# Kernel tuning notes

Hardware: AMD Instinct MI355X
Metric: run time of the kernel (lower is better)

The kernel has to match this reference:

```python
import jax, jax.numpy as jnp
import numpy as np

HIDDEN = 3072
HEADS = 24
HEAD_DIM = HIDDEN // HEADS  # 128
MLP_HIDDEN = 4 * HIDDEN     # 12288
EPS = 1e-6


def rotate_half(x):
    # interleaved pairs: (x1, x2) -> (-x2, x1)
    xr = x.reshape(*x.shape[:-1], -1, 2)
    x1, x2 = xr[..., 0], xr[..., 1]
    return jnp.stack((-x2, x1), axis=-1).reshape(x.shape)


def rms_norm(x, gamma):
    var = jnp.mean(x * x, axis=-1, keepdims=True)
    return x * jax.lax.rsqrt(var + EPS) * gamma


def layer_norm(x):
    mu = jnp.mean(x, axis=-1, keepdims=True)
    var = jnp.mean(jnp.square(x - mu), axis=-1, keepdims=True)
    return (x - mu) * jax.lax.rsqrt(var + EPS)


def setup_inputs() -> dict:
    key = jax.random.key(0)
    ks = jax.random.split(key, 8)
    B, L_IMG, TXT = 2, 1024, 256
    L = L_IMG + TXT
    s = 0.02
    x = jax.random.normal(ks[0], (B, L, HIDDEN), jnp.float32)
    vec = jax.random.normal(ks[1], (B, HIDDEN), jnp.float32)
    w1 = jax.random.normal(ks[2], (HIDDEN, 3 * HIDDEN + MLP_HIDDEN), jnp.float32) * s
    b1 = jnp.zeros((3 * HIDDEN + MLP_HIDDEN,), jnp.float32)
    w2 = jax.random.normal(ks[3], (HIDDEN + MLP_HIDDEN, HIDDEN), jnp.float32) * s
    b2 = jnp.zeros((HIDDEN,), jnp.float32)
    wmod = jax.random.normal(ks[4], (HIDDEN, 3 * HIDDEN), jnp.float32) * s
    bmod = jnp.zeros((3 * HIDDEN,), jnp.float32)
    q_gamma = jnp.ones((HEAD_DIM,), jnp.float32)
    k_gamma = jnp.ones((HEAD_DIM,), jnp.float32)
    # real RoPE tables for the image tokens
    inv_freq = 1.0 / (10000.0 ** (np.arange(0, HEAD_DIM, 2, dtype=np.float32) / HEAD_DIM))
    angles = np.arange(L_IMG, dtype=np.float32)[:, None] * inv_freq[None, :]  # [L_img, D/2]
    freqs_cos = jnp.asarray(np.repeat(np.cos(angles), 2, axis=-1))  # [L_img, D]
    freqs_sin = jnp.asarray(np.repeat(np.sin(angles), 2, axis=-1))
    cu_seqlens_q = jnp.asarray([0, L, L, 2 * L, 2 * L], jnp.int32)  # no padding
    return {"x": x, "vec": vec, "w1": w1, "b1": b1, "w2": w2, "b2": b2,
            "wmod": wmod, "bmod": bmod, "q_gamma": q_gamma, "k_gamma": k_gamma,
            "freqs_cos": freqs_cos, "freqs_sin": freqs_sin,
            "txt_len": TXT, "cu_seqlens_q": cu_seqlens_q}


def reference(x, vec, w1, b1, w2, b2, wmod, bmod, q_gamma, k_gamma,
              freqs_cos, freqs_sin, txt_len, cu_seqlens_q):
    B, L, _ = x.shape
    # modulation: SiLU(vec) @ Wmod -> shift/scale/gate
    mod = jax.nn.silu(vec) @ wmod + bmod              # [B, 3H]
    mod_shift, mod_scale, mod_gate = jnp.split(mod, 3, axis=-1)
    x_mod = layer_norm(x) * (1.0 + mod_scale[:, None, :]) + mod_shift[:, None, :]
    h = x_mod @ w1 + b1                               # [B, L, 3H + mlp]
    qkv, mlp = h[..., :3 * HIDDEN], h[..., 3 * HIDDEN:]
    qkv = qkv.reshape(B, L, 3, HEADS, HEAD_DIM)
    q, k, v = qkv[:, :, 0], qkv[:, :, 1], qkv[:, :, 2]  # [B, L, H, D]
    q = rms_norm(q, q_gamma)
    k = rms_norm(k, k_gamma)
    # RoPE on image tokens (first L - txt_len)
    cos = freqs_cos[None, :, None, :]
    sin = freqs_sin[None, :, None, :]
    img_q, txt_q = q[:, :-txt_len], q[:, -txt_len:]
    img_k, txt_k = k[:, :-txt_len], k[:, -txt_len:]
    img_q = img_q * cos + rotate_half(img_q) * sin
    img_k = img_k * cos + rotate_half(img_k) * sin
    q = jnp.concatenate((img_q, txt_q), axis=1)
    k = jnp.concatenate((img_k, txt_k), axis=1)
    # full attention (no padding => each batch is one varlen segment)
    scale = HEAD_DIM ** -0.5
    scores = jnp.einsum("bqhd,bkhd->bhqk", q, k) * scale
    probs = jax.nn.softmax(scores, axis=-1)
    attn = jnp.einsum("bhqk,bkhd->bqhd", probs, v).reshape(B, L, HIDDEN)
    out = jnp.concatenate((attn, jax.nn.gelu(mlp, approximate=True)), axis=-1) @ w2 + b2
    return x + out * mod_gate[:, None, :]
```

## Files before the change

kernel.cpp:

```cpp
#include <hip/hip_runtime.h>

typedef unsigned short u16;
typedef unsigned int   u32;
typedef __attribute__((ext_vector_type(2))) u16 u16x2;
typedef __attribute__((ext_vector_type(4))) u16 u16x4;
typedef __attribute__((ext_vector_type(8))) u16 u16x8;
typedef __attribute__((ext_vector_type(8))) __bf16 bf16x8;
typedef __attribute__((ext_vector_type(4))) float f32x4;

#define HIDDEN 3072
#define LTOT 1280
#define BATCH 2
#define NROWS (BATCH*LTOT)
#define HEADS 24
#define HD 128
#define N1 21504
#define QKVW 9216
#define MLPW 12288
#define A2W 15360
#define EPSF 1e-6f

__device__ __forceinline__ float b2f(u16 u) {
  union { u32 i; float f; } v; v.i = ((u32)u) << 16; return v.f;
}
__device__ __forceinline__ u16 f2b(float f) {
  union { float f; u32 i; } v; v.f = f;
  u32 r = (v.i + 0x7FFFu + ((v.i >> 16) & 1u)) >> 16;
  return (u16)r;
}
__device__ __forceinline__ float lde(const void* p, size_t i, int f) {
  return f ? b2f(((const u16*)p)[i]) : ((const float*)p)[i];
}
__device__ __forceinline__ void gload16(const void* g, void* l) {
  __builtin_amdgcn_global_load_lds((const __attribute__((address_space(1))) void*)g,
                                   (__attribute__((address_space(3))) void*)l, 16, 0, 0);
}
__device__ __forceinline__ bf16x8 ldf(const u16* p) {
  return __builtin_bit_cast(bf16x8, *(const u16x8*)p);
}
__device__ __forceinline__ float gelu_tanh(float x) {
  float u = 0.7978845608028654f * (x + 0.044715f * x * x * x);
  float e = __expf(2.0f * u);
  float th = 1.0f - 2.0f / (e + 1.0f);
  return 0.5f * x * (1.0f + th);
}

__global__ void detect_kernel(const u16* __restrict__ fcos, int* __restrict__ dflag) {
  if (threadIdx.x == 0 && blockIdx.x == 0) *dflag = (fcos[0] == 0x3F80) ? 1 : 0;
}

__global__ void silu_kernel(const void* __restrict__ vec, float* __restrict__ sv,
                            const int* __restrict__ dflag) {
  int flag = *dflag;
  int i = blockIdx.x * 256 + threadIdx.x;
  if (i < BATCH * HIDDEN) { float x = lde(vec, i, flag); sv[i] = x / (1.0f + __expf(-x)); }
}

__global__ void modmul(const void* __restrict__ wmod, const float* __restrict__ sv,
                       float* __restrict__ modp, const int* __restrict__ dflag) {
  int flag = *dflag;
  int j = blockIdx.x * 256 + threadIdx.x;
  int kc = blockIdx.y;
  float a = 0.f, c = 0.f;
  int k0 = kc * 384;
  for (int k = k0; k < k0 + 384; ++k) {
    float w = lde(wmod, (size_t)k * QKVW + j, flag);
    a += sv[k] * w; c += sv[HIDDEN + k] * w;
  }
  modp[(size_t)kc * 2 * QKVW + j] = a;
  modp[(size_t)kc * 2 * QKVW + QKVW + j] = c;
}

__global__ void modred(const float* __restrict__ modp, const void* __restrict__ bmod,
                       float* __restrict__ mod, const int* __restrict__ dflag) {
  int flag = *dflag;
  int j = blockIdx.x * 256 + threadIdx.x;
  float bv = lde(bmod, j, flag);
  float a = bv, c = bv;
#pragma unroll
  for (int kc = 0; kc < 8; ++kc) {
    a += modp[(size_t)kc * 2 * QKVW + j];
    c += modp[(size_t)kc * 2 * QKVW + QKVW + j];
  }
  mod[j] = a; mod[QKVW + j] = c;
}

__global__ __launch_bounds__(256) void ln_mod_kernel(const void* __restrict__ x,
                                                     const float* __restrict__ mod,
                                                     u16* __restrict__ xmod,
                                                     const int* __restrict__ dflag) {
  int flag = *dflag;
  int row = blockIdx.x;
  int b = row / LTOT;
  int t = threadIdx.x, w = t >> 6, l = t & 63;
  float v[12], sum = 0.0f, sq = 0.0f;
  if (flag) {
    const u16* xr = (const u16*)x + (size_t)row * HIDDEN;
#pragma unroll
    for (int p = 0; p < 3; ++p) {
      u16x4 u = *(const u16x4*)&xr[p * 1024 + t * 4];
#pragma unroll
      for (int i = 0; i < 4; ++i) { float f = b2f(u[i]); v[p * 4 + i] = f; sum += f; sq += f * f; }
    }
  } else {
    const float* xr = (const float*)x + (size_t)row * HIDDEN;
#pragma unroll
    for (int p = 0; p < 3; ++p) {
      f32x4 u = *(const f32x4*)&xr[p * 1024 + t * 4];
#pragma unroll
      for (int i = 0; i < 4; ++i) { float f = u[i]; v[p * 4 + i] = f; sum += f; sq += f * f; }
    }
  }
#pragma unroll
  for (int off = 1; off < 64; off <<= 1) { sum += __shfl_xor(sum, off, 64); sq += __shfl_xor(sq, off, 64); }
  __shared__ float red[2][4];
  if (l == 0) { red[0][w] = sum; red[1][w] = sq; }
  __syncthreads();
  sum = red[0][0] + red[0][1] + red[0][2] + red[0][3];
  sq  = red[1][0] + red[1][1] + red[1][2] + red[1][3];
  float mu = sum / (float)HIDDEN;
  float var = sq / (float)HIDDEN - mu * mu;
  float rs = rsqrtf(var + EPSF);
  const float* mb = mod + (size_t)b * QKVW;
#pragma unroll
  for (int p = 0; p < 3; ++p) {
    u16x4 o;
#pragma unroll
    for (int i = 0; i < 4; ++i) {
      int col = p * 1024 + t * 4 + i;
      float y = (v[p * 4 + i] - mu) * rs;
      o[i] = f2b(y * (1.0f + mb[HIDDEN + col]) + mb[col]);
    }
    *(u16x4*)&xmod[(size_t)row * HIDDEN + p * 1024 + t * 4] = o;
  }
}

__global__ void transpose_cvt(const void* __restrict__ in, u16* __restrict__ out,
                              int R, int C, const int* __restrict__ dflag) {
  int flag = *dflag;
  __shared__ u16 tile[32][33];
  int bx = blockIdx.x * 32, by = blockIdx.y * 32;
  int tx = threadIdx.x & 31, ty = threadIdx.x >> 5;
#pragma unroll
  for (int i = 0; i < 32; i += 8)
    tile[ty + i][tx] = f2b(lde(in, (size_t)(by + ty + i) * C + bx + tx, flag));
  __syncthreads();
#pragma unroll
  for (int i = 0; i < 32; i += 8) out[(size_t)(bx + ty + i) * R + by + tx] = tile[tx][ty + i];
}

__global__ void transpose_bf16(const u16* __restrict__ in, u16* __restrict__ out,
                               int R, int C, size_t ibs, size_t obs) {
  in  += (size_t)blockIdx.z * ibs;
  out += (size_t)blockIdx.z * obs;
  __shared__ u16 tile[32][33];
  int bx = blockIdx.x * 32, by = blockIdx.y * 32;
  int tx = threadIdx.x & 31, ty = threadIdx.x >> 5;
#pragma unroll
  for (int i = 0; i < 32; i += 8) tile[ty + i][tx] = in[(size_t)(by + ty + i) * C + bx + tx];
  __syncthreads();
#pragma unroll
  for (int i = 0; i < 32; i += 8) out[(size_t)(bx + ty + i) * R + by + tx] = tile[tx][ty + i];
}

__global__ __launch_bounds__(512, 2) void gemm1_8ph(
    const u16* __restrict__ A, const u16* __restrict__ Bt,
    const void* __restrict__ bias,
    u16* __restrict__ Qb, u16* __restrict__ Kb, u16* __restrict__ Vb,
    u16* __restrict__ A2, const int* __restrict__ dflag) {
  __shared__ u16 As[2][2][256][32];
  __shared__ u16 Bs[2][2][256][32];
  constexpr int K = HIDDEN;
  constexpr int NT = K / 64;
  const int tid = threadIdx.x;
  const int l = tid & 63, w = tid >> 6;
  const int wr = w >> 2, wc = w & 3;
  const int lr = l & 15, g = l >> 4;
  const int lk_sw = (g ^ ((lr >> 1) & 3)) * 8;

  const int orig = blockIdx.x;
  const int wgid = (orig & 7) * 105 + (orig >> 3);
  const int my = wgid / 84, nx = wgid - my * 84;
  const int bm = my * 256, bn = nx * 256;

  const int row_s = tid >> 2, chunk = tid & 3;
  const int c_log = chunk ^ ((row_s >> 1) & 3);
  const u16* pa = A  + (size_t)(bm + row_s) * K + c_log * 8;
  const u16* pb = Bt + (size_t)(bn + row_s) * K + c_log * 8;

  auto stage_a = [&](int buf, int kk, int t) {
    const u16* sa = pa + kk * 32 + t * 64;
    u16* la = &As[buf][kk][row_s][chunk * 8];
    gload16(sa,                   la);
    gload16(sa + (size_t)128 * K, la + 128 * 32);
  };
  auto stage_b = [&](int buf, int kk, int t) {
    const u16* sb = pb + kk * 32 + t * 64;
    u16* lb = &Bs[buf][kk][row_s][chunk * 8];
    gload16(sb,                   lb);
    gload16(sb + (size_t)128 * K, lb + 128 * 32);
  };

  f32x4 acc[8][4] = {};

  stage_a(0, 0, 0); stage_b(0, 0, 0); stage_a(0, 1, 0); stage_b(0, 1, 0);
  asm volatile("s_waitcnt vmcnt(4)" ::: "memory");
  __builtin_amdgcn_s_barrier();

  bf16x8 af[4], bfr[4];
  for (int t = 0; t < NT; ++t) {
    const int b = t & 1;
    const bool pre = (t + 1 < NT);

#pragma unroll
    for (int fc = 0; fc < 4; ++fc) bfr[fc] = ldf(&Bs[b][0][wc * 64 + fc * 16 + lr][lk_sw]);
#pragma unroll
    for (int j = 0; j < 4; ++j) af[j] = ldf(&As[b][0][wr * 128 + j * 16 + lr][lk_sw]);
    if (pre) stage_a(b ^ 1, 0, t + 1);
    __builtin_amdgcn_s_barrier();
    asm volatile("s_waitcnt lgkmcnt(0)" ::: "memory");
    __builtin_amdgcn_sched_barrier(0);
    __builtin_amdgcn_s_setprio(1);
#pragma unroll
    for (int j = 0; j < 4; ++j)
#pragma unroll
      for (int fc = 0; fc < 4; ++fc)
        acc[j][fc] = __builtin_amdgcn_mfma_f32_16x16x32_bf16(af[j], bfr[fc], acc[j][fc], 0, 0, 0);
    __builtin_amdgcn_s_setprio(0);
    __builtin_amdgcn_s_barrier();

#pragma unroll
    for (int j = 0; j < 4; ++j) af[j] = ldf(&As[b][0][wr * 128 + (4 + j) * 16 + lr][lk_sw]);
    if (pre) stage_b(b ^ 1, 0, t + 1);
    if (pre) { asm volatile("s_waitcnt vmcnt(4)" ::: "memory"); }
    else     { asm volatile("s_waitcnt vmcnt(0)" ::: "memory"); }
    __builtin_amdgcn_s_barrier();
    asm volatile("s_waitcnt lgkmcnt(0)" ::: "memory");
    __builtin_amdgcn_sched_barrier(0);
    __builtin_amdgcn_s_setprio(1);
#pragma unroll
    for (int j = 0; j < 4; ++j)
#pragma unroll
      for (int fc = 0; fc < 4; ++fc)
        acc[4 + j][fc] = __builtin_amdgcn_mfma_f32_16x16x32_bf16(af[j], bfr[fc], acc[4 + j][fc], 0, 0, 0);
    __builtin_amdgcn_s_setprio(0);
    __builtin_amdgcn_s_barrier();

#pragma unroll
    for (int fc = 0; fc < 4; ++fc) bfr[fc] = ldf(&Bs[b][1][wc * 64 + fc * 16 + lr][lk_sw]);
#pragma unroll
    for (int j = 0; j < 4; ++j) af[j] = ldf(&As[b][1][wr * 128 + j * 16 + lr][lk_sw]);
    if (pre) stage_a(b ^ 1, 1, t + 1);
    __builtin_amdgcn_s_barrier();
    asm volatile("s_waitcnt lgkmcnt(0)" ::: "memory");
    __builtin_amdgcn_sched_barrier(0);
    __builtin_amdgcn_s_setprio(1);
#pragma unroll
    for (int j = 0; j < 4; ++j)
#pragma unroll
      for (int fc = 0; fc < 4; ++fc)
        acc[j][fc] = __builtin_amdgcn_mfma_f32_16x16x32_bf16(af[j], bfr[fc], acc[j][fc], 0, 0, 0);
    __builtin_amdgcn_s_setprio(0);
    __builtin_amdgcn_s_barrier();

#pragma unroll
    for (int j = 0; j < 4; ++j) af[j] = ldf(&As[b][1][wr * 128 + (4 + j) * 16 + lr][lk_sw]);
    if (pre) {
      stage_b(b ^ 1, 1, t + 1);
      asm volatile("s_waitcnt vmcnt(4)" ::: "memory");
    }
    __builtin_amdgcn_s_barrier();
    asm volatile("s_waitcnt lgkmcnt(0)" ::: "memory");
    __builtin_amdgcn_sched_barrier(0);
    __builtin_amdgcn_s_setprio(1);
#pragma unroll
    for (int j = 0; j < 4; ++j)
#pragma unroll
      for (int fc = 0; fc < 4; ++fc)
        acc[4 + j][fc] = __builtin_amdgcn_mfma_f32_16x16x32_bf16(af[j], bfr[fc], acc[4 + j][fc], 0, 0, 0);
    __builtin_amdgcn_s_setprio(0);
    __builtin_amdgcn_s_barrier();
  }

  const int flag = *dflag;
#pragma unroll
  for (int fr = 0; fr < 8; ++fr) {
#pragma unroll
    for (int fc = 0; fc < 4; ++fc) {
      int colg = bn + wc * 64 + fc * 16 + lr;
      float bv = lde(bias, colg, flag);
#pragma unroll
      for (int r = 0; r < 4; ++r) {
        int rowg = bm + wr * 128 + fr * 16 + g * 4 + r;
        float v = acc[fr][fc][r] + bv;
        if (colg < QKVW) {
          int which = colg / HIDDEN;
          int hd = colg - which * HIDDEN;
          int h = hd >> 7, d = hd & 127;
          int b2 = rowg / LTOT, pos = rowg - b2 * LTOT;
          u16* dst = (which == 0) ? Qb : ((which == 1) ? Kb : Vb);
          dst[(((size_t)(b2 * HEADS + h)) * LTOT + pos) * HD + d] = f2b(v);
        } else {
          A2[(size_t)rowg * A2W + HIDDEN + (colg - QKVW)] = f2b(gelu_tanh(v));
        }
      }
    }
  }
}

template <int MODE>
__global__ __launch_bounds__(256) void gemm_bt(
    const u16* __restrict__ A, const u16* __restrict__ Bt, int K,
    const void* __restrict__ bias,
    u16* __restrict__ out0, u16* __restrict__ out1, u16* __restrict__ out2,
    u16* __restrict__ out3, float* __restrict__ outf,
    const void* __restrict__ xin, const float* __restrict__ mod,
    const int* __restrict__ dflag) {
  __shared__ u16 As[128 * 32];
  __shared__ u16 Bs[128 * 32];
  const int flag = *dflag;
  const int t = threadIdx.x;
  const int bn = blockIdx.x * 128;
  const int bm = blockIdx.y * 128;
  const int w = t >> 6, l = t & 63;
  const int wr = (w >> 1) * 64, wc = (w & 1) * 64;
  const int lr = l & 15, lk = (l >> 4) * 8;
  f32x4 acc[4][4] = {};
  const size_t a_base = (size_t)bm * K;
  const size_t b_base = (size_t)bn * K;
  const int e0 = t * 8, e1 = e0 + 2048;
  const int r0 = e0 >> 5, c0 = e0 & 31;
  const int r1 = e1 >> 5, c1 = e1 & 31;
  const int nk = K / 32;
  for (int kt = 0; kt < nk; ++kt) {
    const int k0 = kt * 32;
    __syncthreads();
    gload16(A + a_base + (size_t)r0 * K + k0 + c0, (u16*)As + e0);
    gload16(A + a_base + (size_t)r1 * K + k0 + c1, (u16*)As + e1);
    gload16(Bt + b_base + (size_t)r0 * K + k0 + c0, (u16*)Bs + e0);
    gload16(Bt + b_base + (size_t)r1 * K + k0 + c1, (u16*)Bs + e1);
    __syncthreads();
    bf16x8 af[4], bfr[4];
#pragma unroll
    for (int i = 0; i < 4; ++i) {
      af[i]  = __builtin_bit_cast(bf16x8, *(const u16x8*)&As[(wr + i * 16 + lr) * 32 + lk]);
      bfr[i] = __builtin_bit_cast(bf16x8, *(const u16x8*)&Bs[(wc + i * 16 + lr) * 32 + lk]);
    }
#pragma unroll
    for (int i = 0; i < 4; ++i)
#pragma unroll
      for (int j = 0; j < 4; ++j)
        acc[i][j] = __builtin_amdgcn_mfma_f32_16x16x32_bf16(af[i], bfr[j], acc[i][j], 0, 0, 0);
  }
#pragma unroll
  for (int i = 0; i < 4; ++i) {
#pragma unroll
    for (int j = 0; j < 4; ++j) {
      int colg = bn + wc + j * 16 + lr;
      float bv = lde(bias, colg, flag);
#pragma unroll
      for (int r = 0; r < 4; ++r) {
        int rowg = bm + wr + i * 16 + (l >> 4) * 4 + r;
        float v = acc[i][j][r] + bv;
        if (MODE == 1) {
        } else {
          int b = rowg / LTOT;
          float gg = mod[(size_t)b * QKVW + 2 * HIDDEN + colg];
          float xv = lde(xin, (size_t)rowg * HIDDEN + colg, flag);
          outf[(size_t)rowg * HIDDEN + colg] = xv + v * gg;
        }
      }
    }
  }
}

__global__ __launch_bounds__(256) void rms_rope(
    u16* __restrict__ Qb, u16* __restrict__ Kb,
    const void* __restrict__ qg, const void* __restrict__ kg,
    const void* __restrict__ fcos, const void* __restrict__ fsin,
    const int* __restrict__ dflag) {
  int flag = *dflag;
  int w = threadIdx.x >> 6, l = threadIdx.x & 63;
  int rid = blockIdx.x * 4 + w;
  int pos = rid % LTOT;
  int d0 = 2 * l;
  size_t off = (size_t)rid * HD + d0;
  u16x2 qu = *(const u16x2*)&Qb[off];
  u16x2 ku = *(const u16x2*)&Kb[off];
  float q0 = b2f(qu[0]), q1 = b2f(qu[1]);
  float k0 = b2f(ku[0]), k1 = b2f(ku[1]);
  float sq = q0 * q0 + q1 * q1, sk = k0 * k0 + k1 * k1;
#pragma unroll
  for (int o = 1; o < 64; o <<= 1) { sq += __shfl_xor(sq, o, 64); sk += __shfl_xor(sk, o, 64); }
  float rq = rsqrtf(sq / 128.0f + EPSF), rk = rsqrtf(sk / 128.0f + EPSF);
  q0 *= rq * lde(qg, d0, flag); q1 *= rq * lde(qg, d0 + 1, flag);
  k0 *= rk * lde(kg, d0, flag); k1 *= rk * lde(kg, d0 + 1, flag);
  if (pos < 1024) {
    float cc = lde(fcos, (size_t)pos * HD + d0, flag);
    float ss = lde(fsin, (size_t)pos * HD + d0, flag);
    float nq0 = q0 * cc - q1 * ss, nq1 = q1 * cc + q0 * ss;
    float nk0 = k0 * cc - k1 * ss, nk1 = k1 * cc + k0 * ss;
    q0 = nq0; q1 = nq1; k0 = nk0; k1 = nk1;
  }
  u16x2 qo; qo[0] = f2b(q0); qo[1] = f2b(q1);
  u16x2 ko; ko[0] = f2b(k0); ko[1] = f2b(k1);
  *(u16x2*)&Qb[off] = qo;
  *(u16x2*)&Kb[off] = ko;
}

__global__ __launch_bounds__(256) void attn_kernel(
    const u16* __restrict__ Qb, const u16* __restrict__ Kb, const u16* __restrict__ Vt,
    u16* __restrict__ A2) {
  __shared__ u16 Ks[32 * 128];
  __shared__ u16 Vs[128 * 32];
  __shared__ u16 Ps[4][512];
  int t = threadIdx.x, w = t >> 6, l = t & 63;
  int bh = blockIdx.y;
  int q0 = blockIdx.x * 64 + w * 16;
  size_t base = (size_t)bh * LTOT * HD;
  int lr = l & 15, lk = (l >> 4) * 8;
  const float scale = 0.08838834764831845f;

  bf16x8 qf[4];
#pragma unroll
  for (int c = 0; c < 4; ++c)
    qf[c] = __builtin_bit_cast(bf16x8, *(const u16x8*)&Qb[base + (size_t)(q0 + lr) * HD + c * 32 + lk]);

  f32x4 o[8] = {};
  float mrun[4] = {-1e30f, -1e30f, -1e30f, -1e30f};
  float lrun[4] = {0.f, 0.f, 0.f, 0.f};

  const int e0 = t * 8, e1 = e0 + 2048;
  const int vd0 = e0 >> 5, vc0 = e0 & 31;
  const int vd1 = e1 >> 5, vc1 = e1 & 31;

  for (int kt = 0; kt < LTOT / 32; ++kt) {
    __syncthreads();
    gload16(Kb + base + (size_t)kt * 32 * HD + e0, (u16*)Ks + e0);
    gload16(Kb + base + (size_t)kt * 32 * HD + e1, (u16*)Ks + e1);
    gload16(Vt + base + (size_t)vd0 * LTOT + kt * 32 + vc0, (u16*)Vs + e0);
    gload16(Vt + base + (size_t)vd1 * LTOT + kt * 32 + vc1, (u16*)Vs + e1);
    __syncthreads();

    f32x4 s[2] = {};
#pragma unroll
    for (int sb = 0; sb < 2; ++sb)
#pragma unroll
      for (int c = 0; c < 4; ++c) {
        bf16x8 kf = __builtin_bit_cast(bf16x8, *(const u16x8*)&Ks[(sb * 16 + lr) * 128 + c * 32 + lk]);
        s[sb] = __builtin_amdgcn_mfma_f32_16x16x32_bf16(qf[c], kf, s[sb], 0, 0, 0);
      }
#pragma unroll
    for (int sb = 0; sb < 2; ++sb)
#pragma unroll
      for (int j = 0; j < 4; ++j) s[sb][j] *= scale;

#pragma unroll
    for (int j = 0; j < 4; ++j) {
      float mt = fmaxf(s[0][j], s[1][j]);
#pragma unroll
      for (int off = 1; off < 16; off <<= 1) mt = fmaxf(mt, __shfl_xor(mt, off, 64));
      float mnew = fmaxf(mrun[j], mt);
      float f = __expf(mrun[j] - mnew);
      float p0 = __expf(s[0][j] - mnew), p1 = __expf(s[1][j] - mnew);
      float ps = p0 + p1;
#pragma unroll
      for (int off = 1; off < 16; off <<= 1) ps += __shfl_xor(ps, off, 64);
      lrun[j] = lrun[j] * f + ps;
      mrun[j] = mnew;
#pragma unroll
      for (int nb = 0; nb < 8; ++nb) o[nb][j] *= f;
      int prow = (l >> 4) * 4 + j;
      Ps[w][prow * 32 + lr] = f2b(p0);
      Ps[w][prow * 32 + 16 + lr] = f2b(p1);
    }
    __syncthreads();
    bf16x8 pa = __builtin_bit_cast(bf16x8, *(const u16x8*)&Ps[w][lr * 32 + lk]);
#pragma unroll
    for (int nb = 0; nb < 8; ++nb) {
      bf16x8 vf = __builtin_bit_cast(bf16x8, *(const u16x8*)&Vs[(nb * 16 + lr) * 32 + lk]);
      o[nb] = __builtin_amdgcn_mfma_f32_16x16x32_bf16(pa, vf, o[nb], 0, 0, 0);
    }
  }

  int b = bh / HEADS, h = bh % HEADS;
#pragma unroll
  for (int j = 0; j < 4; ++j) {
    float inv = 1.0f / lrun[j];
    size_t row = (size_t)b * LTOT + q0 + (l >> 4) * 4 + j;
#pragma unroll
    for (int nb = 0; nb < 8; ++nb) {
      int col = h * HD + nb * 16 + lr;
      A2[row * A2W + col] = f2b(o[nb][j] * inv);
    }
  }
}

extern "C" void kernel_launch(void* const* d_in, const int* in_sizes, int n_in,
                              void* d_out, int out_size, void* d_ws, size_t ws_size,
                              hipStream_t stream) {
  const void* x    = d_in[0];
  const void* vec  = d_in[1];
  const void* w1   = d_in[2];
  const void* b1   = d_in[3];
  const void* w2   = d_in[4];
  const void* b2   = d_in[5];
  const void* wmod = d_in[6];
  const void* bmod = d_in[7];
  const void* qg   = d_in[8];
  const void* kg   = d_in[9];
  const void* fcos = d_in[10];
  const void* fsin = d_in[11];

  char* p = (char*)d_ws;
  int* dflag  = (int*)p; p += 256;
  float* sv   = (float*)p; p += 32768;
  float* mod  = (float*)p; p += 131072;
  float* modp = (float*)p; p += 8 * 2 * QKVW * 4;
  u16* xmod = (u16*)p; p += (size_t)NROWS * HIDDEN * 2;
  u16* w1t  = (u16*)p; p += (size_t)N1 * HIDDEN * 2;
  u16* Qb   = (u16*)p; p += (size_t)48 * LTOT * HD * 2;
  u16* Kb   = (u16*)p; p += (size_t)48 * LTOT * HD * 2;
  u16* Vb   = (u16*)p; p += (size_t)48 * LTOT * HD * 2;
  u16* Vt   = (u16*)p; p += (size_t)48 * LTOT * HD * 2;
  u16* A2   = (u16*)p; p += (size_t)NROWS * A2W * 2;
  u16* w2t  = w1t;

  detect_kernel<<<1, 64, 0, stream>>>((const u16*)fcos, dflag);
  silu_kernel<<<24, 256, 0, stream>>>(vec, sv, dflag);
  modmul<<<dim3(36, 8), 256, 0, stream>>>(wmod, sv, modp, dflag);
  modred<<<36, 256, 0, stream>>>(modp, bmod, mod, dflag);
  ln_mod_kernel<<<NROWS, 256, 0, stream>>>(x, mod, xmod, dflag);
  transpose_cvt<<<dim3(N1 / 32, HIDDEN / 32), 256, 0, stream>>>(w1, w1t, HIDDEN, N1, dflag);
  gemm1_8ph<<<(N1 / 256) * (NROWS / 256), 512, 0, stream>>>(xmod, w1t, b1,
                                                            Qb, Kb, Vb, A2, dflag);
  rms_rope<<<48 * LTOT / 4, 256, 0, stream>>>(Qb, Kb, qg, kg, fcos, fsin, dflag);
  transpose_bf16<<<dim3(HD / 32, LTOT / 32, 48), 256, 0, stream>>>(Vb, Vt, LTOT, HD,
                                                                   (size_t)LTOT * HD, (size_t)LTOT * HD);
  attn_kernel<<<dim3(LTOT / 64, 48), 256, 0, stream>>>(Qb, Kb, Vt, A2);
  transpose_cvt<<<dim3(HIDDEN / 32, A2W / 32), 256, 0, stream>>>(w2, w2t, A2W, HIDDEN, dflag);
  gemm_bt<2><<<dim3(HIDDEN / 128, NROWS / 128), 256, 0, stream>>>(A2, w2t, A2W, b2,
                                                                  nullptr, nullptr, nullptr, nullptr,
                                                                  (float*)d_out, x, mod, dflag);
}
```

Measured before the change: 1.543 ms.

## Restructure GEMM1 K-loop into triple-buffered 32-wide stages with two-ahead prefetch

Replaces the double-buffered 64-wide K-step pipeline (two 32-wide sub-stages per buffer) in the QKV/MLP projection GEMM with a three-slot ring of 32-wide K tiles, prefetching two iterations ahead. The aim is to give global loads more lead time and hide memory latency behind MFMA work. Shared memory use drops from 4 to 3 tile slots per operand, but each iteration now covers half the K depth, so there are twice as many iterations and barriers, plus modulo-3 buffer indexing.

```diff
diff --git a/kernel.cpp b/kernel.cpp
--- a/kernel.cpp
+++ b/kernel.cpp
@@ -163,15 +163,15 @@
   for (int i = 0; i < 32; i += 8) out[(size_t)(bx + ty + i) * R + by + tx] = tile[tx][ty + i];
 }
 
-__global__ __launch_bounds__(512, 2) void gemm1_8ph(
+__global__ __launch_bounds__(512, 2) void gemm1_p3(
     const u16* __restrict__ A, const u16* __restrict__ Bt,
     const void* __restrict__ bias,
     u16* __restrict__ Qb, u16* __restrict__ Kb, u16* __restrict__ Vb,
     u16* __restrict__ A2, const int* __restrict__ dflag) {
-  __shared__ u16 As[2][2][256][32];
-  __shared__ u16 Bs[2][2][256][32];
+  __shared__ u16 As[3][256][32];
+  __shared__ u16 Bs[3][256][32];
   constexpr int K = HIDDEN;
-  constexpr int NT = K / 64;
+  constexpr int NT = K / 32;
   const int tid = threadIdx.x;
   const int l = tid & 63, w = tid >> 6;
   const int wr = w >> 2, wc = w & 3;
@@ -188,35 +188,38 @@
   const u16* pa = A  + (size_t)(bm + row_s) * K + c_log * 8;
   const u16* pb = Bt + (size_t)(bn + row_s) * K + c_log * 8;
 
-  auto stage_a = [&](int buf, int kk, int t) {
-    const u16* sa = pa + kk * 32 + t * 64;
-    u16* la = &As[buf][kk][row_s][chunk * 8];
+  auto stage_a = [&](int buf, int t) {
+    const u16* sa = pa + t * 32;
+    u16* la = &As[buf][row_s][chunk * 8];
     gload16(sa,                   la);
     gload16(sa + (size_t)128 * K, la + 128 * 32);
   };
-  auto stage_b = [&](int buf, int kk, int t) {
-    const u16* sb = pb + kk * 32 + t * 64;
-    u16* lb = &Bs[buf][kk][row_s][chunk * 8];
+  auto stage_b = [&](int buf, int t) {
+    const u16* sb = pb + t * 32;
+    u16* lb = &Bs[buf][row_s][chunk * 8];
     gload16(sb,                   lb);
     gload16(sb + (size_t)128 * K, lb + 128 * 32);
   };
 
   f32x4 acc[8][4] = {};
 
-  stage_a(0, 0, 0); stage_b(0, 0, 0); stage_a(0, 1, 0); stage_b(0, 1, 0);
-  asm volatile("s_waitcnt vmcnt(4)" ::: "memory");
+  stage_a(0, 0); stage_b(0, 0);
+  stage_a(1, 1); stage_b(1, 1);
+  stage_a(2, 2); stage_b(2, 2);
+  asm volatile("s_waitcnt vmcnt(8)" ::: "memory");
   __builtin_amdgcn_s_barrier();
 
   bf16x8 af[4], bfr[4];
   for (int t = 0; t < NT; ++t) {
-    const int b = t & 1;
-    const bool pre = (t + 1 < NT);
-
-#pragma unroll
-    for (int fc = 0; fc < 4; ++fc) bfr[fc] = ldf(&Bs[b][0][wc * 64 + fc * 16 + lr][lk_sw]);
-#pragma unroll
-    for (int j = 0; j < 4; ++j) af[j] = ldf(&As[b][0][wr * 128 + j * 16 + lr][lk_sw]);
-    if (pre) stage_a(b ^ 1, 0, t + 1);
+    const int buf = t % 3;
+    const int buf2 = (t + 2) % 3;
+    const bool pre = (t + 2 < NT);
+
+#pragma unroll
+    for (int fc = 0; fc < 4; ++fc) bfr[fc] = ldf(&Bs[buf][wc * 64 + fc * 16 + lr][lk_sw]);
+#pragma unroll
+    for (int j = 0; j < 4; ++j) af[j] = ldf(&As[buf][wr * 128 + j * 16 + lr][lk_sw]);
+    if (pre) stage_a(buf2, t + 2);
     __builtin_amdgcn_s_barrier();
     asm volatile("s_waitcnt lgkmcnt(0)" ::: "memory");
     __builtin_amdgcn_sched_barrier(0);
@@ -230,44 +233,12 @@
     __builtin_amdgcn_s_barrier();
 
 #pragma unroll
-    for (int j = 0; j < 4; ++j) af[j] = ldf(&As[b][0][wr * 128 + (4 + j) * 16 + lr][lk_sw]);
-    if (pre) stage_b(b ^ 1, 0, t + 1);
-    if (pre) { asm volatile("s_waitcnt vmcnt(4)" ::: "memory"); }
-    else     { asm volatile("s_waitcnt vmcnt(0)" ::: "memory"); }
-    __builtin_amdgcn_s_barrier();
-    asm volatile("s_waitcnt lgkmcnt(0)" ::: "memory");
-    __builtin_amdgcn_sched_barrier(0);
-    __builtin_amdgcn_s_setprio(1);
-#pragma unroll
-    for (int j = 0; j < 4; ++j)
-#pragma unroll
-      for (int fc = 0; fc < 4; ++fc)
-        acc[4 + j][fc] = __builtin_amdgcn_mfma_f32_16x16x32_bf16(af[j], bfr[fc], acc[4 + j][fc], 0, 0, 0);
-    __builtin_amdgcn_s_setprio(0);
-    __builtin_amdgcn_s_barrier();
-
-#pragma unroll
-    for (int fc = 0; fc < 4; ++fc) bfr[fc] = ldf(&Bs[b][1][wc * 64 + fc * 16 + lr][lk_sw]);
-#pragma unroll
-    for (int j = 0; j < 4; ++j) af[j] = ldf(&As[b][1][wr * 128 + j * 16 + lr][lk_sw]);
-    if (pre) stage_a(b ^ 1, 1, t + 1);
-    __builtin_amdgcn_s_barrier();
-    asm volatile("s_waitcnt lgkmcnt(0)" ::: "memory");
-    __builtin_amdgcn_sched_barrier(0);
-    __builtin_amdgcn_s_setprio(1);
-#pragma unroll
-    for (int j = 0; j < 4; ++j)
-#pragma unroll
-      for (int fc = 0; fc < 4; ++fc)
-        acc[j][fc] = __builtin_amdgcn_mfma_f32_16x16x32_bf16(af[j], bfr[fc], acc[j][fc], 0, 0, 0);
-    __builtin_amdgcn_s_setprio(0);
-    __builtin_amdgcn_s_barrier();
-
-#pragma unroll
-    for (int j = 0; j < 4; ++j) af[j] = ldf(&As[b][1][wr * 128 + (4 + j) * 16 + lr][lk_sw]);
+    for (int j = 0; j < 4; ++j) af[j] = ldf(&As[buf][wr * 128 + (4 + j) * 16 + lr][lk_sw]);
     if (pre) {
-      stage_b(b ^ 1, 1, t + 1);
+      stage_b(buf2, t + 2);
       asm volatile("s_waitcnt vmcnt(4)" ::: "memory");
+    } else if (t + 1 < NT) {
+      asm volatile("s_waitcnt vmcnt(0)" ::: "memory");
     }
     __builtin_amdgcn_s_barrier();
     asm volatile("s_waitcnt lgkmcnt(0)" ::: "memory");
@@ -532,8 +503,8 @@
   modred<<<36, 256, 0, stream>>>(modp, bmod, mod, dflag);
   ln_mod_kernel<<<NROWS, 256, 0, stream>>>(x, mod, xmod, dflag);
   transpose_cvt<<<dim3(N1 / 32, HIDDEN / 32), 256, 0, stream>>>(w1, w1t, HIDDEN, N1, dflag);
-  gemm1_8ph<<<(N1 / 256) * (NROWS / 256), 512, 0, stream>>>(xmod, w1t, b1,
-                                                            Qb, Kb, Vb, A2, dflag);
+  gemm1_p3<<<(N1 / 256) * (NROWS / 256), 512, 0, stream>>>(xmod, w1t, b1,
+                                                           Qb, Kb, Vb, A2, dflag);
   rms_rope<<<48 * LTOT / 4, 256, 0, stream>>>(Qb, Kb, qg, kg, fcos, fsin, dflag);
   transpose_bf16<<<dim3(HD / 32, LTOT / 32, 48), 256, 0, stream>>>(Vb, Vt, LTOT, HD,
                                                                    (size_t)LTOT * HD, (size_t)LTOT * HD);
```

New measurement: 1.477 ms. 1.05x faster.
